# Kernel tuning notes

Hardware: AMD Instinct MI355X
Metric: run time of the kernel (lower is better)

## Reference

```python
import jax, jax.numpy as jnp
import numpy as np

H = 16          # num_attention_heads
DH = 64         # attention_head_size
HID = H * DH    # hidden_size = 1024
EPS = 1e-12


def _layernorm(x, gamma, beta):
    mu = jnp.mean(x, axis=-1, keepdims=True)
    var = jnp.mean(jnp.square(x - mu), axis=-1, keepdims=True)
    return (x - mu) * jax.lax.rsqrt(var + EPS) * gamma + beta


def _attention(q, k, v, mask, Wo, bo, gamma, beta):
    # q,k,v: [B,S,HID] already linearly projected
    B, Tq, _ = q.shape
    Tk = k.shape[1]
    qh = q.reshape(B, Tq, H, DH)
    kh = k.reshape(B, Tk, H, DH)
    vh = v.reshape(B, Tk, H, DH)
    scores = jnp.einsum('bqhd,bkhd->bhqk', qh, kh) / np.sqrt(DH).astype(q.dtype)
    if mask is not None:
        scores = scores + mask  # mask broadcasts [B,1,1,Tk]
    probs = jax.nn.softmax(scores, axis=-1)
    ctx = jnp.einsum('bhqk,bkhd->bqhd', probs, vh)
    proj = jnp.einsum('bqhd,hdo->bqo', ctx, Wo) + bo
    # NOTE: residual is the projected query q (faithful to the source)
    return _layernorm(q + proj, gamma, beta)


def setup_inputs() -> dict:
    key = jax.random.key(0)
    ks = jax.random.split(key, 20)
    B, T, S = 4, 1024, 1024
    s = 0.02
    inp = {
        'encoder_states': jax.random.normal(ks[0], (B, S, HID), jnp.float32),
        'decoder_inputs': jax.random.normal(ks[1], (B, T, HID), jnp.float32),
        'src_attention_mask': jnp.zeros((B, 1, 1, S), jnp.float32),
        'tgt_attention_mask': jnp.zeros((B, 1, 1, T), jnp.float32),
        'Wq': jax.random.normal(ks[2], (HID, HID), jnp.float32) * s,
        'bq': jnp.zeros((HID,), jnp.float32),
        'Wk': jax.random.normal(ks[3], (HID, HID), jnp.float32) * s,
        'bk': jnp.zeros((HID,), jnp.float32),
        'Wv': jax.random.normal(ks[4], (HID, HID), jnp.float32) * s,
        'bv': jnp.zeros((HID,), jnp.float32),
        'Wq2': jax.random.normal(ks[5], (HID, HID), jnp.float32) * s,
        'bq2': jnp.zeros((HID,), jnp.float32),
        'Wk2': jax.random.normal(ks[6], (HID, HID), jnp.float32) * s,
        'bk2': jnp.zeros((HID,), jnp.float32),
        'Wv2': jax.random.normal(ks[7], (HID, HID), jnp.float32) * s,
        'bv2': jnp.zeros((HID,), jnp.float32),
        'Wo': jax.random.normal(ks[8], (H, DH, HID), jnp.float32) * s,
        'bo': jnp.zeros((HID,), jnp.float32),
        'gamma': jnp.ones((HID,), jnp.float32),
        'beta': jnp.zeros((HID,), jnp.float32),
    }
    return inp


def reference(encoder_states, decoder_inputs, src_attention_mask, tgt_attention_mask,
              Wq, bq, Wk, bk, Wv, bv, Wq2, bq2, Wk2, bk2, Wv2, bv2,
              Wo, bo, gamma, beta):
    # self-attention over decoder inputs
    q1 = decoder_inputs @ Wq + bq
    k1 = decoder_inputs @ Wk + bk
    v1 = decoder_inputs @ Wv + bv
    self_out = _attention(q1, k1, v1, tgt_attention_mask, Wo, bo, gamma, beta)
    # cross-attention: query from self_out, key/value from encoder states
    q2 = self_out @ Wq2 + bq2
    k2 = encoder_states @ Wk2 + bk2
    v2 = encoder_states @ Wv2 + bv2
    return _attention(q2, k2, v2, src_attention_mask, Wo, bo, gamma, beta)
```

## Files before the change

kernel.cpp:

```cpp
#include <hip/hip_runtime.h>
#include <stdint.h>


typedef unsigned short u16;
typedef __bf16 bf16x8 __attribute__((ext_vector_type(8)));
typedef float f32x4 __attribute__((ext_vector_type(4)));

#define AS1 __attribute__((address_space(1)))
#define AS3 __attribute__((address_space(3)))

#define VMCNT(n) asm volatile("s_waitcnt vmcnt(" #n ")" ::: "memory")
#define SBARRIER() asm volatile("s_barrier" ::: "memory")

__device__ __forceinline__ u16 f2bf(float f) {
  union { float f; uint32_t u; } v; v.f = f;
  uint32_t u = v.u;
  return (u16)((u + 0x7fffu + ((u >> 16) & 1u)) >> 16);
}

__device__ __forceinline__ uint32_t cvt_pk_bf16(float lo, float hi) {
  uint32_t r;
  asm("v_cvt_pk_bf16_f32 %0, %1, %2" : "=v"(r) : "v"(lo), "v"(hi));
  return r;
}

__device__ __forceinline__ void gl_lds16(const void* g, void* l) {
  __builtin_amdgcn_global_load_lds((AS1 void*)(g), (AS3 void*)(l), 16, 0, 0);
}

__device__ __forceinline__ int swz(int row, int byte) {
  return row * 128 + (byte ^ ((row & 7) << 4));
}

__global__ void __launch_bounds__(256)
convert2_kernel(const float* __restrict__ in0, u16* __restrict__ out0,
                const float* __restrict__ in1, u16* __restrict__ out1) {
  const int half = blockIdx.x >> 12;
  const int i = (blockIdx.x & 4095) * 256 + threadIdx.x;
  const float* in = half ? in1 : in0;
  u16* out = half ? out1 : out0;
  float4 v = ((const float4*)in)[i];
  ushort4 o;
  o.x = f2bf(v.x); o.y = f2bf(v.y); o.z = f2bf(v.z); o.w = f2bf(v.w);
  ((ushort4*)out)[i] = o;
}

struct WP { const float* w[7]; };

__global__ void __launch_bounds__(256)
transpose_kernel(WP wp, u16* __restrict__ out) {
  __shared__ float tile[64][65];
  const float* W = wp.w[blockIdx.z];
  u16* Wt = out + (size_t)blockIdx.z * 1024 * 1024;
  const int k0 = blockIdx.y * 64, n0 = blockIdx.x * 64;
  const int t = threadIdx.x;
  const int r = t >> 4, c4 = (t & 15) * 4;
#pragma unroll
  for (int rr = 0; rr < 64; rr += 16) {
    float4 v = *(const float4*)&W[(size_t)(k0 + r + rr) * 1024 + n0 + c4];
    tile[r + rr][c4 + 0] = v.x; tile[r + rr][c4 + 1] = v.y;
    tile[r + rr][c4 + 2] = v.z; tile[r + rr][c4 + 3] = v.w;
  }
  __syncthreads();
  const int n = t >> 2, seg = (t & 3) * 16;
  union { u16 s[16]; uint4 q[2]; } u;
#pragma unroll
  for (int i = 0; i < 16; ++i) u.s[i] = f2bf(tile[seg + i][n]);
  uint4* dst = (uint4*)&Wt[(size_t)(n0 + n) * 1024 + k0 + seg];
  dst[0] = u.q[0]; dst[1] = u.q[1];
}

__global__ void __launch_bounds__(512, 2)
qkv256_kernel(const u16* __restrict__ A0, const u16* __restrict__ A1,
              const u16* __restrict__ A2, const u16* __restrict__ Bt,
              const float* __restrict__ b0, const float* __restrict__ b1,
              const float* __restrict__ b2,
              u16* __restrict__ qb, float* __restrict__ qf,
              u16* __restrict__ kb, u16* __restrict__ vt) {
  __shared__ u16 Alds[2][256 * 32];
  __shared__ u16 Blds[2][256 * 32];
  const int bm = blockIdx.y * 256, bn = blockIdx.x * 256;
  const int seg = bn >> 10;
  const u16* A = (seg == 0) ? A0 : (seg == 1) ? A1 : A2;
  const int t = threadIdx.x, wv = t >> 6, ln = t & 63;
  const int wm = (wv >> 2) * 128, wn = (wv & 3) * 64;
  const int lcol = ln & 15, lk8 = (ln >> 4) * 8, lr4 = (ln >> 4) * 4;

  f32x4 acc[8][4] = {};

  auto STAGE = [&](int buf, int k0) {
#pragma unroll
    for (int c = 0; c < 2; ++c) {
      const int o = c * 8192 + wv * 1024 + ln * 16;
      const int row = o >> 6, colb = o & 63;
      gl_lds16((const char*)A + ((size_t)(bm + row) * 1024 + k0) * 2 + colb,
               (char*)Alds[buf] + c * 8192 + wv * 1024);
      gl_lds16((const char*)Bt + ((size_t)(bn + row) * 1024 + k0) * 2 + colb,
               (char*)Blds[buf] + c * 8192 + wv * 1024);
    }
  };

  auto COMPUTE = [&](int buf) {
    const u16* Ab = Alds[buf];
    const u16* Bb = Blds[buf];
    bf16x8 a[8], b[4];
#pragma unroll
    for (int j = 0; j < 4; ++j)
      b[j] = *(const bf16x8*)&Bb[(wn + j * 16 + lcol) * 32 + lk8];
#pragma unroll
    for (int i = 0; i < 8; ++i)
      a[i] = *(const bf16x8*)&Ab[(wm + i * 16 + lcol) * 32 + lk8];
#pragma unroll
    for (int i = 0; i < 8; ++i)
#pragma unroll
      for (int j = 0; j < 4; ++j)
        acc[i][j] = __builtin_amdgcn_mfma_f32_16x16x32_bf16(a[i], b[j], acc[i][j], 0, 0, 0);
  };

  STAGE(0, 0);
  int cur = 0;
  for (int it = 0; it < 31; ++it) {
    STAGE(cur ^ 1, (it + 1) * 32);
    VMCNT(4);
    SBARRIER();
    COMPUTE(cur);
    SBARRIER();
    cur ^= 1;
  }
  VMCNT(0);
  SBARRIER();
  COMPUTE(cur);

  const int cs = bn & 1023;
  const float* bias = (seg == 0) ? b0 : (seg == 1) ? b1 : b2;
#pragma unroll
  for (int j = 0; j < 4; ++j) {
    const int col = cs + wn + j * 16 + lcol;
    const float bc = bias[col];
#pragma unroll
    for (int i = 0; i < 8; ++i) {
      const int row0 = bm + wm + i * 16 + lr4;
      if (seg == 2) {
        ushort4 o;
        o.x = f2bf(acc[i][j][0] + bc); o.y = f2bf(acc[i][j][1] + bc);
        o.z = f2bf(acc[i][j][2] + bc); o.w = f2bf(acc[i][j][3] + bc);
        const int b_ = row0 >> 10, s = row0 & 1023;
        const int h = col >> 6, d = col & 63;
        *(ushort4*)&vt[(((size_t)(b_ * 16 + h) * 64 + d) << 10) + s] = o;
      } else if (seg == 0) {
#pragma unroll
        for (int r = 0; r < 4; ++r) {
          const size_t idx = (size_t)(row0 + r) * 1024 + col;
          const float v = acc[i][j][r] + bc;
          qb[idx] = f2bf(v); qf[idx] = v;
        }
      } else {
#pragma unroll
        for (int r = 0; r < 4; ++r) {
          const size_t idx = (size_t)(row0 + r) * 1024 + col;
          kb[idx] = f2bf(acc[i][j][r] + bc);
        }
      }
    }
  }
}

__global__ void __launch_bounds__(256)
gemm_proj(const u16* __restrict__ A, const u16* __restrict__ Bt,
          const float* __restrict__ bias, const float* __restrict__ resid,
          float* __restrict__ outf) {
  __shared__ u16 Alds[2][8192];
  __shared__ u16 Blds[2][8192];
  const int bm = blockIdx.y * 128, bn = blockIdx.x * 128;
  const int t = threadIdx.x, wv = t >> 6, ln = t & 63;
  const int wm = (wv >> 1) * 64, wn = (wv & 1) * 64;
  const int lcol = ln & 15, lk8 = (ln >> 4) * 8, lr4 = (ln >> 4) * 4;

  f32x4 acc[4][4] = {};

  auto STAGE = [&](int buf, int k0) {
#pragma unroll
    for (int c = 0; c < 4; ++c) {
      const int o = c * 4096 + wv * 1024 + ln * 16;
      const int row = o >> 7, colb = o & 127;
      gl_lds16((const char*)A + ((size_t)(bm + row) * 1024 + k0) * 2 + colb,
               (char*)Alds[buf] + c * 4096 + wv * 1024);
      gl_lds16((const char*)Bt + ((size_t)(bn + row) * 1024 + k0) * 2 + colb,
               (char*)Blds[buf] + c * 4096 + wv * 1024);
    }
  };

  auto COMPUTE = [&](int buf) {
    const u16* Ab = Alds[buf];
    const u16* Bb = Blds[buf];
#pragma unroll
    for (int ks = 0; ks < 2; ++ks) {
      bf16x8 a[4], b[4];
#pragma unroll
      for (int i = 0; i < 4; ++i)
        a[i] = *(const bf16x8*)&Ab[(wm + i * 16 + lcol) * 64 + ks * 32 + lk8];
#pragma unroll
      for (int j = 0; j < 4; ++j)
        b[j] = *(const bf16x8*)&Bb[(wn + j * 16 + lcol) * 64 + ks * 32 + lk8];
#pragma unroll
      for (int i = 0; i < 4; ++i)
#pragma unroll
        for (int j = 0; j < 4; ++j)
          acc[i][j] = __builtin_amdgcn_mfma_f32_16x16x32_bf16(a[i], b[j], acc[i][j], 0, 0, 0);
    }
  };

  STAGE(0, 0);
  int cur = 0;
  for (int it = 0; it < 15; ++it) {
    STAGE(cur ^ 1, (it + 1) * 64);
    VMCNT(8);
    SBARRIER();
    COMPUTE(cur);
    SBARRIER();
    cur ^= 1;
  }
  VMCNT(0);
  SBARRIER();
  COMPUTE(cur);

#pragma unroll
  for (int j = 0; j < 4; ++j) {
    const int col = bn + wn + j * 16 + lcol;
    const float bc = bias[col];
#pragma unroll
    for (int i = 0; i < 4; ++i) {
      const int row0 = bm + wm + i * 16 + lr4;
#pragma unroll
      for (int r = 0; r < 4; ++r) {
        const size_t idx = (size_t)(row0 + r) * 1024 + col;
        outf[idx] = acc[i][j][r] + bc + resid[idx];
      }
    }
  }
}

__global__ void __launch_bounds__(256)
attn_kernel(const u16* __restrict__ Q, const u16* __restrict__ Kb,
            const u16* __restrict__ Vt, const float* __restrict__ mask,
            u16* __restrict__ ctx) {
  __shared__ u16 Klds[2][64 * 64];
  __shared__ u16 Vlds[2][64 * 64];
  __shared__ u16 Plds[4][16 * 64];

  const int fid = blockIdx.x;
  const int xcd = fid & 7, idx = fid >> 3;
  const int bh = xcd * 8 + (idx >> 4);
  const int b = bh >> 4, h = bh & 15;
  const int q0 = (idx & 15) * 64;

  const int t = threadIdx.x, wv = t >> 6, ln = t & 63;
  const int lcol = ln & 15, g = ln >> 4;
  const int lk8 = g * 8, c0 = g * 16;

  const int qrow = q0 + wv * 16 + lcol;
  const u16* qptr = Q + ((size_t)(b * 1024 + qrow) * 1024 + h * 64);
  bf16x8 qa[2];
  qa[0] = *(const bf16x8*)(qptr + lk8);
  qa[1] = *(const bf16x8*)(qptr + 32 + lk8);

  const float* mrow = mask + b * 1024;
  char* pbase = (char*)&Plds[wv][0];

  f32x4 accO[4] = {};
  float m_r = -1e30f, l_r = 0.f;

  auto STAGE = [&](int buf, int s0) {
#pragma unroll
    for (int c = 0; c < 2; ++c) {
      const int o = c * 4096 + wv * 1024 + ln * 16;
      const int row = o >> 7;
      const int src_cb = (o & 127) ^ ((row & 7) << 4);
      gl_lds16((const char*)Kb + ((size_t)((b * 1024 + s0 + row) * 1024 + h * 64)) * 2 + src_cb,
               (char*)Klds[buf] + c * 4096 + wv * 1024);
      gl_lds16((const char*)Vt + ((size_t)(((b * 16 + h) * 64 + row) * 1024 + s0)) * 2 + src_cb,
               (char*)Vlds[buf] + c * 4096 + wv * 1024);
    }
  };

  auto TILE = [&](int buf, const float4* mk) {
    f32x4 accST[4] = {};
    __builtin_amdgcn_s_setprio(1);
#pragma unroll
    for (int ks = 0; ks < 2; ++ks)
#pragma unroll
      for (int sb = 0; sb < 4; ++sb) {
        bf16x8 kb = *(const bf16x8*)((const char*)Klds[buf] + swz(sb * 16 + lcol, ks * 64 + c0));
        accST[sb] = __builtin_amdgcn_mfma_f32_16x16x32_bf16(kb, qa[ks], accST[sb], 0, 0, 0);
      }
    __builtin_amdgcn_s_setprio(0);

    float sv[4][4];
#pragma unroll
    for (int sb = 0; sb < 4; ++sb) {
      sv[sb][0] = accST[sb][0] * 0.125f + mk[sb].x;
      sv[sb][1] = accST[sb][1] * 0.125f + mk[sb].y;
      sv[sb][2] = accST[sb][2] * 0.125f + mk[sb].z;
      sv[sb][3] = accST[sb][3] * 0.125f + mk[sb].w;
    }
    float mt = sv[0][0];
#pragma unroll
    for (int sb = 0; sb < 4; ++sb)
#pragma unroll
      for (int r = 0; r < 4; ++r) mt = fmaxf(mt, sv[sb][r]);
    mt = fmaxf(mt, __shfl_xor(mt, 16));
    mt = fmaxf(mt, __shfl_xor(mt, 32));

    const float mn = fmaxf(m_r, mt);
    const float alpha = __expf(m_r - mn);
    m_r = mn;
    float rs = 0.f;
#pragma unroll
    for (int sb = 0; sb < 4; ++sb)
#pragma unroll
      for (int r = 0; r < 4; ++r) {
        const float pp = __expf(sv[sb][r] - mn);
        sv[sb][r] = pp;
        rs += pp;
      }
    rs += __shfl_xor(rs, 16);
    rs += __shfl_xor(rs, 32);
    l_r = l_r * alpha + rs;

#pragma unroll
    for (int sb = 0; sb < 4; ++sb) {
      uint2 dd;
      dd.x = cvt_pk_bf16(sv[sb][0], sv[sb][1]);
      dd.y = cvt_pk_bf16(sv[sb][2], sv[sb][3]);
      *(uint2*)(pbase + swz(lcol, sb * 32 + g * 8)) = dd;
    }

#pragma unroll
    for (int df = 0; df < 4; ++df)
#pragma unroll
      for (int r = 0; r < 4; ++r) accO[df][r] *= alpha;
    __builtin_amdgcn_s_setprio(1);
#pragma unroll
    for (int ks = 0; ks < 2; ++ks) {
      bf16x8 pb = *(const bf16x8*)(pbase + swz(lcol, ks * 64 + c0));
#pragma unroll
      for (int df = 0; df < 4; ++df) {
        bf16x8 va = *(const bf16x8*)((const char*)Vlds[buf] + swz(df * 16 + lcol, ks * 64 + c0));
        accO[df] = __builtin_amdgcn_mfma_f32_16x16x32_bf16(va, pb, accO[df], 0, 0, 0);
      }
    }
    __builtin_amdgcn_s_setprio(0);
  };

  STAGE(0, 0);
  float4 mk_cur[4];
#pragma unroll
  for (int sb = 0; sb < 4; ++sb)
    mk_cur[sb] = *(const float4*)&mrow[sb * 16 + g * 4];

  int cur = 0;
  for (int ti = 0; ti < 15; ++ti) {
    const int s1 = ti * 64 + 64;
    STAGE(cur ^ 1, s1);
    float4 mk_nxt[4];
#pragma unroll
    for (int sb = 0; sb < 4; ++sb)
      mk_nxt[sb] = *(const float4*)&mrow[s1 + sb * 16 + g * 4];
    VMCNT(12);
    SBARRIER();
    TILE(cur, mk_cur);
    SBARRIER();
#pragma unroll
    for (int sb = 0; sb < 4; ++sb) mk_cur[sb] = mk_nxt[sb];
    cur ^= 1;
  }
  VMCNT(4);
  SBARRIER();
  TILE(cur, mk_cur);

  const float inv = 1.0f / l_r;
  u16* cp = ctx + ((size_t)(b * 1024 + qrow) * 1024 + h * 64);
#pragma unroll
  for (int df = 0; df < 4; ++df) {
    ushort4 o;
    o.x = f2bf(accO[df][0] * inv); o.y = f2bf(accO[df][1] * inv);
    o.z = f2bf(accO[df][2] * inv); o.w = f2bf(accO[df][3] * inv);
    *(ushort4*)(cp + df * 16 + g * 4) = o;
  }
}

template <int OUTF>
__global__ void __launch_bounds__(256)
ln_kernel(const float* __restrict__ x, const float* __restrict__ gamma,
          const float* __restrict__ beta, float* __restrict__ outf,
          u16* __restrict__ outb) {
  const int row = blockIdx.x, t = threadIdx.x;
  const float* xr = x + (size_t)row * 1024;
  float4 v = *(const float4*)&xr[t * 4];
  float s = v.x + v.y + v.z + v.w;
  float q = v.x * v.x + v.y * v.y + v.z * v.z + v.w * v.w;
#pragma unroll
  for (int off = 1; off < 64; off <<= 1) {
    s += __shfl_xor(s, off);
    q += __shfl_xor(q, off);
  }
  __shared__ float ws[4], wq[4];
  if ((t & 63) == 0) { ws[t >> 6] = s; wq[t >> 6] = q; }
  __syncthreads();
  s = ws[0] + ws[1] + ws[2] + ws[3];
  q = wq[0] + wq[1] + wq[2] + wq[3];
  const float mu = s * (1.0f / 1024.0f);
  float var = q * (1.0f / 1024.0f) - mu * mu;
  var = fmaxf(var, 0.0f);
  const float rstd = rsqrtf(var + 1e-12f);
  float4 g = *(const float4*)&gamma[t * 4];
  float4 be = *(const float4*)&beta[t * 4];
  float y0 = (v.x - mu) * rstd * g.x + be.x;
  float y1 = (v.y - mu) * rstd * g.y + be.y;
  float y2 = (v.z - mu) * rstd * g.z + be.z;
  float y3 = (v.w - mu) * rstd * g.w + be.w;
  if constexpr (OUTF) {
    float4 o; o.x = y0; o.y = y1; o.z = y2; o.w = y3;
    *(float4*)&outf[(size_t)row * 1024 + t * 4] = o;
  } else {
    ushort4 o; o.x = f2bf(y0); o.y = f2bf(y1); o.z = f2bf(y2); o.w = f2bf(y3);
    *(ushort4*)&outb[(size_t)row * 1024 + t * 4] = o;
  }
}

extern "C" void kernel_launch(void* const* d_in, const int* in_sizes, int n_in,
                              void* d_out, int out_size, void* d_ws, size_t ws_size,
                              hipStream_t stream) {
  const float* enc = (const float*)d_in[0];
  const float* dec = (const float*)d_in[1];
  const float* src_mask = (const float*)d_in[2];
  const float* tgt_mask = (const float*)d_in[3];
  const float* Wq  = (const float*)d_in[4];  const float* bq  = (const float*)d_in[5];
  const float* Wk  = (const float*)d_in[6];  const float* bk  = (const float*)d_in[7];
  const float* Wv  = (const float*)d_in[8];  const float* bv  = (const float*)d_in[9];
  const float* Wq2 = (const float*)d_in[10]; const float* bq2 = (const float*)d_in[11];
  const float* Wk2 = (const float*)d_in[12]; const float* bk2 = (const float*)d_in[13];
  const float* Wv2 = (const float*)d_in[14]; const float* bv2 = (const float*)d_in[15];
  const float* Wo  = (const float*)d_in[16]; const float* bo  = (const float*)d_in[17];
  const float* gamma = (const float*)d_in[18]; const float* beta = (const float*)d_in[19];
  float* out = (float*)d_out;

  char* p = (char*)d_ws;
  const size_t ABF = (size_t)4096 * 1024 * 2;
  const size_t AF  = (size_t)4096 * 1024 * 4;
  const size_t WBF = (size_t)1024 * 1024 * 2;
  u16* decbf = (u16*)p; p += ABF;
  u16* encbf = (u16*)p; p += ABF;
  u16* wt    = (u16*)p; p += 7 * WBF;
  u16* qbf   = (u16*)p; p += ABF;
  float* qf  = (float*)p; p += AF;
  u16* kbf   = (u16*)p; p += ABF;
  u16* vtb   = (u16*)p; p += ABF;
  u16* ctxb  = (u16*)p; p += ABF;
  float* tmpf = (float*)p; p += AF;
  u16* sobf  = decbf;

  u16* WoT  = wt + 6 * 1048576;

  dim3 b256(256);
  convert2_kernel<<<8192, b256, 0, stream>>>(dec, decbf, enc, encbf);
  WP wp;
  wp.w[0] = Wq; wp.w[1] = Wk; wp.w[2] = Wv; wp.w[3] = Wq2;
  wp.w[4] = Wk2; wp.w[5] = Wv2; wp.w[6] = Wo;
  transpose_kernel<<<dim3(16, 16, 7), b256, 0, stream>>>(wp, wt);

  qkv256_kernel<<<dim3(12, 16), 512, 0, stream>>>(
      decbf, decbf, decbf, wt, bq, bk, bv, qbf, qf, kbf, vtb);
  attn_kernel<<<1024, b256, 0, stream>>>(qbf, kbf, vtb, tgt_mask, ctxb);
  gemm_proj<<<dim3(8, 32), b256, 0, stream>>>(ctxb, WoT, bo, qf, tmpf);
  ln_kernel<0><<<4096, b256, 0, stream>>>(tmpf, gamma, beta, nullptr, sobf);
  qkv256_kernel<<<dim3(12, 16), 512, 0, stream>>>(
      sobf, encbf, encbf, wt + 3 * 1048576, bq2, bk2, bv2, qbf, qf, kbf, vtb);
  attn_kernel<<<1024, b256, 0, stream>>>(qbf, kbf, vtb, src_mask, ctxb);
  gemm_proj<<<dim3(8, 32), b256, 0, stream>>>(ctxb, WoT, bo, qf, tmpf);
  ln_kernel<1><<<4096, b256, 0, stream>>>(tmpf, gamma, beta, out, nullptr);
}
```

Before: 259.1 us.

## Pipeline QKV GEMM with 4-stage LDS ring, drop fp32 Q copy, lazy softmax rescale

The QKV GEMM now uses a 4-buffer LDS ring with split A/B staging interleaved between two half-tile MFMA phases. It adds swizzled LDS reads through inline ds_read_b128, priority hints and an XCD-aware block remap. The fp32 query copy is removed, so the output projection reads the bf16 query as its residual, cutting global writes and reads at some cost in residual precision. gemm_proj also gets a block-index remap for cache locality. Attention skips the running-max rescale while the new block max stays within 8 of the old one, saving exps and multiplies but risking overflow in extreme cases.

```diff
diff --git a/kernel.cpp b/kernel.cpp
--- a/kernel.cpp
+++ b/kernel.cpp
@@ -8,8 +8,11 @@
 
 #define AS1 __attribute__((address_space(1)))
 #define AS3 __attribute__((address_space(3)))
+typedef AS3 char lds_char;
+typedef AS3 unsigned short lds_u16;
 
 #define VMCNT(n) asm volatile("s_waitcnt vmcnt(" #n ")" ::: "memory")
+#define LGKM0() asm volatile("s_waitcnt lgkmcnt(0)" ::: "memory")
 #define SBARRIER() asm volatile("s_barrier" ::: "memory")
 
 __device__ __forceinline__ u16 f2bf(float f) {
@@ -18,6 +21,11 @@
   return (u16)((u + 0x7fffu + ((u >> 16) & 1u)) >> 16);
 }
 
+__device__ __forceinline__ float bf2f(u16 b) {
+  union { uint32_t u; float f; } v; v.u = ((uint32_t)b) << 16;
+  return v.f;
+}
+
 __device__ __forceinline__ uint32_t cvt_pk_bf16(float lo, float hi) {
   uint32_t r;
   asm("v_cvt_pk_bf16_f32 %0, %1, %2" : "=v"(r) : "v"(lo), "v"(hi));
@@ -26,6 +34,12 @@
 
 __device__ __forceinline__ void gl_lds16(const void* g, void* l) {
   __builtin_amdgcn_global_load_lds((AS1 void*)(g), (AS3 void*)(l), 16, 0, 0);
+}
+
+__device__ __forceinline__ bf16x8 dsr128(const lds_u16* p) {
+  bf16x8 r;
+  asm volatile("ds_read_b128 %0, %1" : "=v"(r) : "v"(p));
+  return r;
 }
 
 __device__ __forceinline__ int swz(int row, int byte) {
@@ -71,68 +85,106 @@
 }
 
 __global__ void __launch_bounds__(512, 2)
-qkv256_kernel(const u16* __restrict__ A0, const u16* __restrict__ A1,
-              const u16* __restrict__ A2, const u16* __restrict__ Bt,
-              const float* __restrict__ b0, const float* __restrict__ b1,
-              const float* __restrict__ b2,
-              u16* __restrict__ qb, float* __restrict__ qf,
-              u16* __restrict__ kb, u16* __restrict__ vt) {
-  __shared__ u16 Alds[2][256 * 32];
-  __shared__ u16 Blds[2][256 * 32];
-  const int bm = blockIdx.y * 256, bn = blockIdx.x * 256;
-  const int seg = bn >> 10;
+qkv4b_kernel(const u16* __restrict__ A0, const u16* __restrict__ A1,
+             const u16* __restrict__ A2, const u16* __restrict__ Bt,
+             const float* __restrict__ b0, const float* __restrict__ b1,
+             const float* __restrict__ b2,
+             u16* __restrict__ qb, u16* __restrict__ kb, u16* __restrict__ vt) {
+  __shared__ u16 Alds[4][256 * 32];
+  __shared__ u16 Blds[4][256 * 32];
+
+  const int d = blockIdx.y * 12 + blockIdx.x;
+  const int c = d & 7, ci = d >> 3;
+  const int mt = (c & 3) * 4 + (ci & 3);
+  const int nt = (c >> 2) * 6 + (ci >> 2);
+  const int bm = mt * 256, bn = nt * 256;
+  const int seg = nt >> 2;
   const u16* A = (seg == 0) ? A0 : (seg == 1) ? A1 : A2;
+
   const int t = threadIdx.x, wv = t >> 6, ln = t & 63;
   const int wm = (wv >> 2) * 128, wn = (wv & 3) * 64;
-  const int lcol = ln & 15, lk8 = (ln >> 4) * 8, lr4 = (ln >> 4) * 4;
+  const int lcol = ln & 15, g = ln >> 4, lr4 = g * 4;
+  const int aoff = (g * 16) ^ ((lcol & 3) << 4);
+
+  lds_char* ABase = (lds_char*)&Alds[0][0];
+  lds_char* BBase = (lds_char*)&Blds[0][0];
+
+  const int st_row = wv * 16 + (ln >> 2);
+  const int st_srcb = (((ln & 3) ^ ((ln >> 2) & 3)) * 16);
+  auto stageA = [&](int buf, int k0) {
+#pragma unroll
+    for (int hf = 0; hf < 2; ++hf) {
+      const int row = hf * 128 + st_row;
+      gl_lds16((const char*)A + ((size_t)(bm + row) * 1024 + k0) * 2 + st_srcb,
+               (char*)ABase + buf * 16384 + hf * 8192 + wv * 1024);
+    }
+  };
+  auto stageB = [&](int buf, int k0) {
+#pragma unroll
+    for (int hf = 0; hf < 2; ++hf) {
+      const int row = hf * 128 + st_row;
+      gl_lds16((const char*)Bt + ((size_t)(bn + row) * 1024 + k0) * 2 + st_srcb,
+               (char*)BBase + buf * 16384 + hf * 8192 + wv * 1024);
+    }
+  };
 
   f32x4 acc[8][4] = {};
 
-  auto STAGE = [&](int buf, int k0) {
-#pragma unroll
-    for (int c = 0; c < 2; ++c) {
-      const int o = c * 8192 + wv * 1024 + ln * 16;
-      const int row = o >> 6, colb = o & 63;
-      gl_lds16((const char*)A + ((size_t)(bm + row) * 1024 + k0) * 2 + colb,
-               (char*)Alds[buf] + c * 8192 + wv * 1024);
-      gl_lds16((const char*)Bt + ((size_t)(bn + row) * 1024 + k0) * 2 + colb,
-               (char*)Blds[buf] + c * 8192 + wv * 1024);
-    }
-  };
-
-  auto COMPUTE = [&](int buf) {
-    const u16* Ab = Alds[buf];
-    const u16* Bb = Blds[buf];
-    bf16x8 a[8], b[4];
+  stageA(0, 0); stageB(0, 0);
+  stageA(1, 32); stageB(1, 32);
+  VMCNT(4);
+  __builtin_amdgcn_s_barrier();
+
+  for (int kt = 0; kt < 32; ++kt) {
+    const int buf = kt & 3;
+    lds_char* Ab = ABase + buf * 16384;
+    lds_char* Bb = BBase + buf * 16384;
+    const int sbuf = (kt + 2) & 3;
+    const int sk = (kt + 2) * 32;
+    const bool do_st = kt < 30;
+    bf16x8 afr[4], bfr[4];
+
 #pragma unroll
     for (int j = 0; j < 4; ++j)
-      b[j] = *(const bf16x8*)&Bb[(wn + j * 16 + lcol) * 32 + lk8];
-#pragma unroll
-    for (int i = 0; i < 8; ++i)
-      a[i] = *(const bf16x8*)&Ab[(wm + i * 16 + lcol) * 32 + lk8];
-#pragma unroll
-    for (int i = 0; i < 8; ++i)
+      bfr[j] = dsr128((const lds_u16*)(Bb + (wn + j * 16 + lcol) * 64 + aoff));
+#pragma unroll
+    for (int i = 0; i < 4; ++i)
+      afr[i] = dsr128((const lds_u16*)(Ab + (wm + i * 16 + lcol) * 64 + aoff));
+    if (do_st) stageA(sbuf, sk);
+    __builtin_amdgcn_s_barrier();
+    LGKM0();
+    __builtin_amdgcn_sched_barrier(0);
+    __builtin_amdgcn_s_setprio(1);
+#pragma unroll
+    for (int i = 0; i < 4; ++i)
 #pragma unroll
       for (int j = 0; j < 4; ++j)
-        acc[i][j] = __builtin_amdgcn_mfma_f32_16x16x32_bf16(a[i], b[j], acc[i][j], 0, 0, 0);
-  };
-
-  STAGE(0, 0);
-  int cur = 0;
-  for (int it = 0; it < 31; ++it) {
-    STAGE(cur ^ 1, (it + 1) * 32);
-    VMCNT(4);
-    SBARRIER();
-    COMPUTE(cur);
-    SBARRIER();
-    cur ^= 1;
-  }
-  VMCNT(0);
-  SBARRIER();
-  COMPUTE(cur);
+        acc[i][j] = __builtin_amdgcn_mfma_f32_16x16x32_bf16(afr[i], bfr[j], acc[i][j], 0, 0, 0);
+    __builtin_amdgcn_s_setprio(0);
+    __builtin_amdgcn_s_barrier();
+
+#pragma unroll
+    for (int i = 0; i < 4; ++i)
+      afr[i] = dsr128((const lds_u16*)(Ab + (wm + 64 + i * 16 + lcol) * 64 + aoff));
+    if (do_st) stageB(sbuf, sk);
+    __builtin_amdgcn_s_barrier();
+    LGKM0();
+    __builtin_amdgcn_sched_barrier(0);
+    __builtin_amdgcn_s_setprio(1);
+#pragma unroll
+    for (int i = 0; i < 4; ++i)
+#pragma unroll
+      for (int j = 0; j < 4; ++j)
+        acc[4 + i][j] = __builtin_amdgcn_mfma_f32_16x16x32_bf16(afr[i], bfr[j], acc[4 + i][j], 0, 0, 0);
+    __builtin_amdgcn_s_setprio(0);
+    if (kt < 30) { VMCNT(4); }
+    else if (kt == 30) { VMCNT(0); }
+    __builtin_amdgcn_s_barrier();
+  }
 
   const int cs = bn & 1023;
   const float* bias = (seg == 0) ? b0 : (seg == 1) ? b1 : b2;
+  u16* outp = (seg == 0) ? qb : kb;
 #pragma unroll
   for (int j = 0; j < 4; ++j) {
     const int col = cs + wn + j * 16 + lcol;
@@ -145,21 +197,12 @@
         o.x = f2bf(acc[i][j][0] + bc); o.y = f2bf(acc[i][j][1] + bc);
         o.z = f2bf(acc[i][j][2] + bc); o.w = f2bf(acc[i][j][3] + bc);
         const int b_ = row0 >> 10, s = row0 & 1023;
-        const int h = col >> 6, d = col & 63;
-        *(ushort4*)&vt[(((size_t)(b_ * 16 + h) * 64 + d) << 10) + s] = o;
-      } else if (seg == 0) {
-#pragma unroll
-        for (int r = 0; r < 4; ++r) {
-          const size_t idx = (size_t)(row0 + r) * 1024 + col;
-          const float v = acc[i][j][r] + bc;
-          qb[idx] = f2bf(v); qf[idx] = v;
-        }
+        const int h = col >> 6, dd = col & 63;
+        *(ushort4*)&vt[(((size_t)(b_ * 16 + h) * 64 + dd) << 10) + s] = o;
       } else {
 #pragma unroll
-        for (int r = 0; r < 4; ++r) {
-          const size_t idx = (size_t)(row0 + r) * 1024 + col;
-          kb[idx] = f2bf(acc[i][j][r] + bc);
-        }
+        for (int r = 0; r < 4; ++r)
+          outp[(size_t)(row0 + r) * 1024 + col] = f2bf(acc[i][j][r] + bc);
       }
     }
   }
@@ -167,11 +210,15 @@
 
 __global__ void __launch_bounds__(256)
 gemm_proj(const u16* __restrict__ A, const u16* __restrict__ Bt,
-          const float* __restrict__ bias, const float* __restrict__ resid,
+          const float* __restrict__ bias, const u16* __restrict__ resid,
           float* __restrict__ outf) {
   __shared__ u16 Alds[2][8192];
   __shared__ u16 Blds[2][8192];
-  const int bm = blockIdx.y * 128, bn = blockIdx.x * 128;
+  const int d = blockIdx.y * 8 + blockIdx.x;
+  const int c = d & 7, ci = d >> 3;
+  const int mt = (c & 3) * 8 + (ci & 7);
+  const int nt = (c >> 2) * 4 + (ci >> 3);
+  const int bm = mt * 128, bn = nt * 128;
   const int t = threadIdx.x, wv = t >> 6, ln = t & 63;
   const int wm = (wv >> 1) * 64, wn = (wv & 1) * 64;
   const int lcol = ln & 15, lk8 = (ln >> 4) * 8, lr4 = (ln >> 4) * 4;
@@ -180,13 +227,13 @@
 
   auto STAGE = [&](int buf, int k0) {
 #pragma unroll
-    for (int c = 0; c < 4; ++c) {
-      const int o = c * 4096 + wv * 1024 + ln * 16;
+    for (int cc = 0; cc < 4; ++cc) {
+      const int o = cc * 4096 + wv * 1024 + ln * 16;
       const int row = o >> 7, colb = o & 127;
       gl_lds16((const char*)A + ((size_t)(bm + row) * 1024 + k0) * 2 + colb,
-               (char*)Alds[buf] + c * 4096 + wv * 1024);
+               (char*)Alds[buf] + cc * 4096 + wv * 1024);
       gl_lds16((const char*)Bt + ((size_t)(bn + row) * 1024 + k0) * 2 + colb,
-               (char*)Blds[buf] + c * 4096 + wv * 1024);
+               (char*)Blds[buf] + cc * 4096 + wv * 1024);
     }
   };
 
@@ -234,7 +281,7 @@
 #pragma unroll
       for (int r = 0; r < 4; ++r) {
         const size_t idx = (size_t)(row0 + r) * 1024 + col;
-        outf[idx] = acc[i][j][r] + bc + resid[idx];
+        outf[idx] = acc[i][j][r] + bc + bf2f(resid[idx]);
       }
     }
   }
@@ -311,21 +358,25 @@
     mt = fmaxf(mt, __shfl_xor(mt, 16));
     mt = fmaxf(mt, __shfl_xor(mt, 32));
 
-    const float mn = fmaxf(m_r, mt);
-    const float alpha = __expf(m_r - mn);
-    m_r = mn;
+    const bool nr = __all(mt <= m_r + 8.0f) != 0;
+    float alpha = 1.0f;
+    if (!nr) {
+      const float mn2 = fmaxf(m_r, mt);
+      alpha = __expf(m_r - mn2);
+      m_r = mn2;
+    }
     float rs = 0.f;
 #pragma unroll
     for (int sb = 0; sb < 4; ++sb)
 #pragma unroll
       for (int r = 0; r < 4; ++r) {
-        const float pp = __expf(sv[sb][r] - mn);
+        const float pp = __expf(sv[sb][r] - m_r);
         sv[sb][r] = pp;
         rs += pp;
       }
     rs += __shfl_xor(rs, 16);
     rs += __shfl_xor(rs, 32);
-    l_r = l_r * alpha + rs;
+    l_r = nr ? (l_r + rs) : (l_r * alpha + rs);
 
 #pragma unroll
     for (int sb = 0; sb < 4; ++sb) {
@@ -335,10 +386,12 @@
       *(uint2*)(pbase + swz(lcol, sb * 32 + g * 8)) = dd;
     }
 
-#pragma unroll
-    for (int df = 0; df < 4; ++df)
-#pragma unroll
-      for (int r = 0; r < 4; ++r) accO[df][r] *= alpha;
+    if (!nr) {
+#pragma unroll
+      for (int df = 0; df < 4; ++df)
+#pragma unroll
+        for (int r = 0; r < 4; ++r) accO[df][r] *= alpha;
+    }
     __builtin_amdgcn_s_setprio(1);
 #pragma unroll
     for (int ks = 0; ks < 2; ++ks) {
@@ -453,7 +506,6 @@
   u16* encbf = (u16*)p; p += ABF;
   u16* wt    = (u16*)p; p += 7 * WBF;
   u16* qbf   = (u16*)p; p += ABF;
-  float* qf  = (float*)p; p += AF;
   u16* kbf   = (u16*)p; p += ABF;
   u16* vtb   = (u16*)p; p += ABF;
   u16* ctxb  = (u16*)p; p += ABF;
@@ -469,14 +521,14 @@
   wp.w[4] = Wk2; wp.w[5] = Wv2; wp.w[6] = Wo;
   transpose_kernel<<<dim3(16, 16, 7), b256, 0, stream>>>(wp, wt);
 
-  qkv256_kernel<<<dim3(12, 16), 512, 0, stream>>>(
-      decbf, decbf, decbf, wt, bq, bk, bv, qbf, qf, kbf, vtb);
+  qkv4b_kernel<<<dim3(12, 16), 512, 0, stream>>>(
+      decbf, decbf, decbf, wt, bq, bk, bv, qbf, kbf, vtb);
   attn_kernel<<<1024, b256, 0, stream>>>(qbf, kbf, vtb, tgt_mask, ctxb);
-  gemm_proj<<<dim3(8, 32), b256, 0, stream>>>(ctxb, WoT, bo, qf, tmpf);
+  gemm_proj<<<dim3(8, 32), b256, 0, stream>>>(ctxb, WoT, bo, qbf, tmpf);
   ln_kernel<0><<<4096, b256, 0, stream>>>(tmpf, gamma, beta, nullptr, sobf);
-  qkv256_kernel<<<dim3(12, 16), 512, 0, stream>>>(
-      sobf, encbf, encbf, wt + 3 * 1048576, bq2, bk2, bv2, qbf, qf, kbf, vtb);
+  qkv4b_kernel<<<dim3(12, 16), 512, 0, stream>>>(
+      sobf, encbf, encbf, wt + 3 * 1048576, bq2, bk2, bv2, qbf, kbf, vtb);
   attn_kernel<<<1024, b256, 0, stream>>>(qbf, kbf, vtb, src_mask, ctxb);
-  gemm_proj<<<dim3(8, 32), b256, 0, stream>>>(ctxb, WoT, bo, qf, tmpf);
+  gemm_proj<<<dim3(8, 32), b256, 0, stream>>>(ctxb, WoT, bo, qbf, tmpf);
   ln_kernel<1><<<4096, b256, 0, stream>>>(tmpf, gamma, beta, out, nullptr);
 }
```

Measured after the change: 234.2 us. -9.6%, faster.
